# Optimization experiments

Measured on AMD Instinct MI355X. Metric: run time of the kernel, lower is better.

## Reference

```python
import jax, jax.numpy as jnp
import numpy as np

D_MODEL = 1024
N_HEADS = 16
D_K = D_MODEL // N_HEADS  # 64
B, T = 2, 2048


def setup_inputs() -> dict:
    key = jax.random.key(0)
    ks = jax.random.split(key, 6)
    s = 0.02
    x = jax.random.normal(ks[0], (B, T, D_MODEL), dtype=jnp.float32)
    # Stacked per-head projection weights, [H, C, d_k] (no bias, mini-gpt style)
    Wq = jax.random.normal(ks[1], (N_HEADS, D_MODEL, D_K), dtype=jnp.float32) * s
    Wk = jax.random.normal(ks[2], (N_HEADS, D_MODEL, D_K), dtype=jnp.float32) * s
    Wv = jax.random.normal(ks[3], (N_HEADS, D_MODEL, D_K), dtype=jnp.float32) * s
    # Output projection, torch nn.Linear(d_model, d_model): y = x @ Wo.T + bo
    Wo = jax.random.normal(ks[4], (D_MODEL, D_MODEL), dtype=jnp.float32) * s
    bo = jax.random.normal(ks[5], (D_MODEL,), dtype=jnp.float32) * s
    return {"x": x, "Wq": Wq, "Wk": Wk, "Wv": Wv, "Wo": Wo, "bo": bo}


def reference(x, Wq, Wk, Wv, Wo, bo):
    Bq, Tq, C = x.shape
    # Batched per-head projections (replaces the per-head Python loop)
    q = jnp.einsum('btc,hck->bhtk', x, Wq)  # [B,H,T,dk]
    k = jnp.einsum('btc,hck->bhtk', x, Wk)
    v = jnp.einsum('btc,hck->bhtk', x, Wv)
    scale = 1.0 / jnp.sqrt(jnp.asarray(D_K, dtype=x.dtype))
    scores = jnp.einsum('bhtk,bhsk->bhts', q, k) * scale  # [B,H,T,T]
    causal = jnp.tril(jnp.ones((Tq, Tq), dtype=bool))
    scores = jnp.where(causal, scores, jnp.asarray(-1e9, dtype=scores.dtype))
    attn = jax.nn.softmax(scores, axis=-1)
    out = jnp.einsum('bhts,bhsk->bhtk', attn, v)  # [B,H,T,dk]
    # concat heads -> [B,T,C]
    out = out.transpose(0, 2, 1, 3).reshape(Bq, Tq, C)
    return jnp.einsum('btc,dc->btd', out, Wo) + bo
```

## Files before the change

### kernel.cpp

```cpp
#include <hip/hip_runtime.h>
#include <hip/hip_bf16.h>


using short8 = __attribute__((ext_vector_type(8))) short;
using f32x4  = __attribute__((ext_vector_type(4))) float;
using fp16x2 = __attribute__((ext_vector_type(2))) __fp16;
using half4  = __attribute__((ext_vector_type(4))) _Float16;
using half8  = __attribute__((ext_vector_type(8))) _Float16;

#define SCALE_LOG2E 0.18033688011112042f

__device__ __forceinline__ unsigned short f2bf(float f) {
    union { float f; unsigned u; } v; v.f = f;
    unsigned r = v.u + 0x7fffu + ((v.u >> 16) & 1u);
    return (unsigned short)(r >> 16);
}

__device__ __forceinline__ void gld16(const unsigned short* gp, unsigned short* lp) {
    __builtin_amdgcn_global_load_lds(
        (const __attribute__((address_space(1))) void*)(gp),
        (__attribute__((address_space(3))) void*)(unsigned int)(unsigned long long)(lp),
        16, 0, 0);
}

__global__ void prep(const float* __restrict__ x,
                     const float* __restrict__ Wq,
                     const float* __restrict__ Wk,
                     const float* __restrict__ Wv,
                     const float* __restrict__ Wo,
                     unsigned short* __restrict__ xb,
                     unsigned short* __restrict__ wfrag,
                     unsigned short* __restrict__ wofrag) {
    __shared__ float tile[64][65];
    int blk = blockIdx.x;
    int t = threadIdx.x;
    if (blk < 768) {
        int b = blk;
        int cchunk = b & 15;
        int h = (b >> 4) & 15;
        int s = b >> 8;
        const float* W = (s == 0) ? Wq : ((s == 1) ? Wk : Wv);
        float sc = (s == 0) ? SCALE_LOG2E : 1.0f;
        const float* src = W + (h * 1024 + cchunk * 64) * 64;
        #pragma unroll
        for (int it = 0; it < 4; ++it) {
            int idx = (it * 256 + t) * 4;
            int cc = idx >> 6, kk = idx & 63;
            float4 v = *(const float4*)(src + idx);
            tile[cc][kk + 0] = v.x; tile[cc][kk + 1] = v.y;
            tile[cc][kk + 2] = v.z; tile[cc][kk + 3] = v.w;
        }
        __syncthreads();
        int sh = s * 16 + h;
        #pragma unroll
        for (int p = 0; p < 2; ++p) {
            int slot = p * 256 + t;
            int d   = slot & 63;
            int cc8 = slot >> 6;
            int n16  = sh * 4 + (d >> 4);
            int col  = d & 15;
            int kq   = cchunk * 2 + (cc8 >> 2);
            int quad = cc8 & 3;
            ushort4 lo, hi;
            lo.x = f2bf(tile[cc8 * 8 + 0][d] * sc); lo.y = f2bf(tile[cc8 * 8 + 1][d] * sc);
            lo.z = f2bf(tile[cc8 * 8 + 2][d] * sc); lo.w = f2bf(tile[cc8 * 8 + 3][d] * sc);
            hi.x = f2bf(tile[cc8 * 8 + 4][d] * sc); hi.y = f2bf(tile[cc8 * 8 + 5][d] * sc);
            hi.z = f2bf(tile[cc8 * 8 + 6][d] * sc); hi.w = f2bf(tile[cc8 * 8 + 7][d] * sc);
            unsigned short* dst = wfrag + ((size_t)((n16 * 32 + kq) * 64 + quad * 16 + col)) * 8;
            *(ushort4*)dst = lo;
            *(ushort4*)(dst + 4) = hi;
        }
    } else if (blk < 1280) {
        int g = (blk - 768) * 256 + t;
        int col  = g & 15;
        int quad = (g >> 4) & 3;
        int kq   = (g >> 6) & 31;
        int n16  = g >> 11;
        const float* src = Wo + (size_t)(n16 * 16 + col) * 1024 + kq * 32 + quad * 8;
        float4 a = *(const float4*)src;
        float4 b2 = *(const float4*)(src + 4);
        ushort4 lo, hi;
        lo.x = f2bf(a.x); lo.y = f2bf(a.y); lo.z = f2bf(a.z); lo.w = f2bf(a.w);
        hi.x = f2bf(b2.x); hi.y = f2bf(b2.y); hi.z = f2bf(b2.z); hi.w = f2bf(b2.w);
        *(ushort4*)(wofrag + (size_t)g * 8)     = lo;
        *(ushort4*)(wofrag + (size_t)g * 8 + 4) = hi;
    } else {
        int i = (blk - 1280) * 256 + t;
        if (i < 1048576) {
            float4 v = ((const float4*)x)[i];
            ushort4 o;
            o.x = f2bf(v.x); o.y = f2bf(v.y); o.z = f2bf(v.z); o.w = f2bf(v.w);
            ((ushort4*)xb)[i] = o;
        }
    }
}

__global__ __launch_bounds__(128, 4) void qkv_gemm(
        const unsigned short* __restrict__ xb,
        const unsigned short* __restrict__ wtf,
        unsigned short* __restrict__ qB,
        unsigned short* __restrict__ kfrag,
        _Float16* __restrict__ vfrag) {
    __shared__ unsigned short Als[64 * 32];
    int wave = threadIdx.x >> 6;
    int lane = threadIdx.x & 63;
    int col  = lane & 15;
    int quad = lane >> 4;
    int ldr = lane >> 2;
    int ldc = ((lane & 3) ^ ((lane >> 3) & 3)) * 8;
    int swq = (quad ^ ((col >> 1) & 3)) * 8;
    int m0 = blockIdx.x * 64;
    int n0 = blockIdx.y * 128 + wave * 64;
    int n16b = n0 >> 4;
    f32x4 acc[4][4] = {};
    for (int k0 = 0; k0 < 1024; k0 += 32) {
        int kq = k0 >> 5;
        __syncthreads();
        short8 bf[4];
        #pragma unroll
        for (int nb = 0; nb < 4; ++nb)
            bf[nb] = *(const short8*)(wtf +
                ((size_t)((n16b + nb) * 32 + kq) * 64 + lane) * 8);
        #pragma unroll
        for (int j = 0; j < 2; ++j) {
            int row = wave * 32 + j * 16;
            gld16(xb + (size_t)(m0 + row + ldr) * 1024 + k0 + ldc, Als + row * 32);
        }
        __syncthreads();
        short8 af[4];
        #pragma unroll
        for (int i = 0; i < 4; ++i)
            af[i] = *(const short8*)(Als + (i * 16 + col) * 32 + swq);
        #pragma unroll
        for (int mb = 0; mb < 4; ++mb)
            #pragma unroll
            for (int nb = 0; nb < 4; ++nb)
                acc[mb][nb] = __builtin_amdgcn_mfma_f32_16x16x32_bf16(
                    af[mb], bf[nb], acc[mb][nb], 0, 0, 0);
    }
    int sel = blockIdx.y >> 3;
    #pragma unroll
    for (int nb = 0; nb < 4; ++nb) {
        int n = n0 + nb * 16 + col;
        int d10 = n & 1023;
        int h_ = d10 >> 6, d = d10 & 63;
        if (sel == 0) {
            #pragma unroll
            for (int mb = 0; mb < 4; ++mb)
                #pragma unroll
                for (int r = 0; r < 4; ++r) {
                    int m = m0 + mb * 16 + quad * 4 + r;
                    int b_ = m >> 11, t_ = m & 2047;
                    qB[((size_t)(b_ * 16 + h_) * 2048 + t_) * 64 + d] =
                        f2bf(acc[mb][nb][r]);
                }
        } else if (sel == 1) {
            int hK = d >> 5, quadk = (d >> 3) & 3, j = d & 7;
            #pragma unroll
            for (int mb = 0; mb < 4; ++mb)
                #pragma unroll
                for (int r = 0; r < 4; ++r) {
                    int m = m0 + mb * 16 + quad * 4 + r;
                    int b_ = m >> 11, t_ = m & 2047;
                    int bh = b_ * 16 + h_;
                    kfrag[((((size_t)bh * 128 + (t_ >> 4)) * 2 + hK) * 64 +
                           quadk * 16 + (t_ & 15)) * 8 + j] = f2bf(acc[mb][nb][r]);
                }
        } else {
            int nbv = d >> 4, colv = d & 15;
            #pragma unroll
            for (int mb = 0; mb < 4; ++mb) {
                int m = m0 + mb * 16 + quad * 4;
                int b_ = m >> 11, t_ = m & 2047;
                int bh = b_ * 16 + h_;
                half4 hv;
                hv[0] = (_Float16)acc[mb][nb][0]; hv[1] = (_Float16)acc[mb][nb][1];
                hv[2] = (_Float16)acc[mb][nb][2]; hv[3] = (_Float16)acc[mb][nb][3];
                *(half4*)(vfrag + ((((size_t)bh * 64 + (t_ >> 5)) * 4 + nbv) * 64 +
                          ((t_ >> 2) & 3) * 16 + colv) * 8 + ((t_ >> 4) & 1) * 4) = hv;
            }
        }
    }
}

__global__ __launch_bounds__(128, 4) void oproj(
        const unsigned short* __restrict__ A,
        const unsigned short* __restrict__ wof,
        const float* __restrict__ bo,
        float* __restrict__ y) {
    __shared__ unsigned short Als[32 * 32];
    int wave = threadIdx.x >> 6;
    int lane = threadIdx.x & 63;
    int col  = lane & 15;
    int quad = lane >> 4;
    int ldr = lane >> 2;
    int ldc = ((lane & 3) ^ ((lane >> 3) & 3)) * 8;
    int swq = (quad ^ ((col >> 1) & 3)) * 8;
    int m0 = blockIdx.x * 32;
    int n0 = blockIdx.y * 128 + wave * 64;
    int n16b = n0 >> 4;
    f32x4 acc[2][4] = {};
    for (int k0 = 0; k0 < 1024; k0 += 32) {
        int kq = k0 >> 5;
        __syncthreads();
        short8 bf[4];
        #pragma unroll
        for (int nb = 0; nb < 4; ++nb)
            bf[nb] = *(const short8*)(wof +
                ((size_t)((n16b + nb) * 32 + kq) * 64 + lane) * 8);
        gld16(A + (size_t)(m0 + wave * 16 + ldr) * 1024 + k0 + ldc,
              Als + (wave * 16) * 32);
        __syncthreads();
        short8 af[2];
        #pragma unroll
        for (int i = 0; i < 2; ++i)
            af[i] = *(const short8*)(Als + (i * 16 + col) * 32 + swq);
        #pragma unroll
        for (int mb = 0; mb < 2; ++mb)
            #pragma unroll
            for (int nb = 0; nb < 4; ++nb)
                acc[mb][nb] = __builtin_amdgcn_mfma_f32_16x16x32_bf16(
                    af[mb], bf[nb], acc[mb][nb], 0, 0, 0);
    }
    #pragma unroll
    for (int nb = 0; nb < 4; ++nb) {
        int n = n0 + nb * 16 + col;
        float bias = bo[n];
        #pragma unroll
        for (int mb = 0; mb < 2; ++mb)
            #pragma unroll
            for (int r = 0; r < 4; ++r) {
                int m = m0 + mb * 16 + quad * 4 + r;
                y[(size_t)m * 1024 + n] = acc[mb][nb][r] + bias;
            }
    }
}

__global__ __launch_bounds__(256, 3) void attn(
        const unsigned short* __restrict__ qB,
        const unsigned short* __restrict__ kfrag,
        const _Float16* __restrict__ vfrag,
        unsigned short* __restrict__ aout) {
    __shared__ float O_comb[2][64][33];
    __shared__ float L_comb[2][2][2][16];
    int wave = threadIdx.x >> 6;
    int lane = threadIdx.x & 63;
    int col  = lane & 15;
    int quad = lane >> 4;
    int sl     = wave >> 1;
    int parity = wave & 1;
    int bh   = blockIdx.x & 31;
    int pairidx = 31 - (blockIdx.x >> 5);
    int strip = pairidx * 2 + sl;
    int q0 = strip * 32;
    const unsigned short* q = qB + (size_t)bh * 2048 * 64;
    const unsigned short* kf_base = kfrag + (size_t)bh * 128 * 2 * 512;
    const _Float16*       vf_base = vfrag + (size_t)bh * 64 * 4 * 512;

    short8 qf[2][2];
    #pragma unroll
    for (int qb = 0; qb < 2; ++qb)
        #pragma unroll
        for (int h = 0; h < 2; ++h)
            qf[qb][h] = *(const short8*)(q + (size_t)(q0 + qb * 16 + col) * 64 + h * 32 + quad * 8);

    f32x4 o[2][4] = {};
    float l[2] = {0.f, 0.f};

    struct KV { short8 kf[2][2]; half8 vv[4]; };
    KV bufA, bufB;

    auto load_half = [&](int it, int kv32, KV& b) {
        int K16 = it * 4 + kv32 * 2;
        #pragma unroll
        for (int p = 0; p < 2; ++p)
            #pragma unroll
            for (int h = 0; h < 2; ++h)
                b.kf[p][h] = *(const short8*)(kf_base +
                    (((size_t)(K16 + p) * 2 + h) * 64 + lane) * 8);
        #pragma unroll
        for (int nb = 0; nb < 4; ++nb)
            b.vv[nb] = *(const half8*)(vf_base +
                (((size_t)(it * 2 + kv32) * 4 + nb) * 64 + lane) * 8);
    };

    auto compute_half = [&](int it, int kv32, KV& b) {
        int kv0 = it * 64;
        bool diag = (kv0 + 63 > q0);
        #pragma unroll
        for (int par = 0; par < 2; ++par) {
            int kvbase = kv0 + kv32 * 32 + par * 16;
            f32x4 st[2] = {};
            #pragma unroll
            for (int qb = 0; qb < 2; ++qb) {
                st[qb] = __builtin_amdgcn_mfma_f32_16x16x32_bf16(b.kf[par][0], qf[qb][0], st[qb], 0, 0, 0);
                st[qb] = __builtin_amdgcn_mfma_f32_16x16x32_bf16(b.kf[par][1], qf[qb][1], st[qb], 0, 0, 0);
            }
            #pragma unroll
            for (int qb = 0; qb < 2; ++qb) {
                float p0 = __builtin_amdgcn_exp2f(st[qb][0]);
                float p1 = __builtin_amdgcn_exp2f(st[qb][1]);
                float p2 = __builtin_amdgcn_exp2f(st[qb][2]);
                float p3 = __builtin_amdgcn_exp2f(st[qb][3]);
                if (diag) {
                    int qg  = q0 + qb * 16 + col;
                    int kvg = kvbase + quad * 4;
                    p0 = (kvg + 0 > qg) ? 0.f : p0;
                    p1 = (kvg + 1 > qg) ? 0.f : p1;
                    p2 = (kvg + 2 > qg) ? 0.f : p2;
                    p3 = (kvg + 3 > qg) ? 0.f : p3;
                }
                l[qb] += (p0 + p1) + (p2 + p3);
                union { fp16x2 h2[2]; half4 h4; } cvt;
                cvt.h2[0] = __builtin_amdgcn_cvt_pkrtz(p0, p1);
                cvt.h2[1] = __builtin_amdgcn_cvt_pkrtz(p2, p3);
                half4 pf = cvt.h4;
                #pragma unroll
                for (int nb = 0; nb < 4; ++nb) {
                    half4 vf = (par == 0)
                        ? __builtin_shufflevector(b.vv[nb], b.vv[nb], 0, 1, 2, 3)
                        : __builtin_shufflevector(b.vv[nb], b.vv[nb], 4, 5, 6, 7);
                    o[qb][nb] = __builtin_amdgcn_mfma_f32_16x16x16f16(pf, vf, o[qb][nb], 0, 0, 0);
                }
            }
        }
    };

    int n_iter = (q0 + 95) >> 6;
    if (parity < n_iter) load_half(parity, 0, bufA);
    for (int it = parity; it < n_iter; it += 2) {
        load_half(it, 1, bufB);
        compute_half(it, 0, bufA);
        if (it + 2 < n_iter) load_half(it + 2, 0, bufA);
        compute_half(it, 1, bufB);
    }

    #pragma unroll
    for (int qb = 0; qb < 2; ++qb) {
        float lr = l[qb];
        lr += __shfl_xor(lr, 16);
        lr += __shfl_xor(lr, 32);
        l[qb] = lr;
    }
    if (quad == 0) {
        L_comb[sl][parity][0][col] = l[0];
        L_comb[sl][parity][1][col] = l[1];
    }
    if (parity == 1) {
        #pragma unroll
        for (int qb = 0; qb < 2; ++qb)
            #pragma unroll
            for (int nb = 0; nb < 4; ++nb)
                #pragma unroll
                for (int r = 0; r < 4; ++r)
                    O_comb[sl][lane][qb * 16 + nb * 4 + r] = o[qb][nb][r];
    }
    __syncthreads();
    if (parity == 0) {
        int b_ = bh >> 4, h_ = bh & 15;
        #pragma unroll
        for (int qb = 0; qb < 2; ++qb)
            #pragma unroll
            for (int r = 0; r < 4; ++r) {
                int qi = quad * 4 + r;
                float inv_l = 1.0f / (L_comb[sl][0][qb][qi] + L_comb[sl][1][qb][qi]);
                int t_ = q0 + qb * 16 + qi;
                #pragma unroll
                for (int nb = 0; nb < 4; ++nb) {
                    float ov = o[qb][nb][r] + O_comb[sl][lane][qb * 16 + nb * 4 + r];
                    aout[(size_t)(b_ * 2048 + t_) * 1024 + h_ * 64 + nb * 16 + col] =
                        f2bf(ov * inv_l);
                }
            }
    }
}

extern "C" void kernel_launch(void* const* d_in, const int* in_sizes, int n_in,
                              void* d_out, int out_size, void* d_ws, size_t ws_size,
                              hipStream_t stream) {
    const float* x  = (const float*)d_in[0];
    const float* Wq = (const float*)d_in[1];
    const float* Wk = (const float*)d_in[2];
    const float* Wv = (const float*)d_in[3];
    const float* Wo = (const float*)d_in[4];
    const float* bo = (const float*)d_in[5];
    float* y = (float*)d_out;

    unsigned short* xb    = (unsigned short*)d_ws;
    unsigned short* Wtf   = xb    + 4194304;
    unsigned short* Wof   = Wtf   + 3145728;
    unsigned short* qBb   = Wof   + 1048576;
    unsigned short* kfr   = qBb   + 4194304;
    unsigned short* vfr   = kfr   + 4194304;
    unsigned short* aout  = vfr   + 4194304;

    prep<<<5376, 256, 0, stream>>>(x, Wq, Wk, Wv, Wo, xb, Wtf, Wof);
    qkv_gemm<<<dim3(64, 24), 128, 0, stream>>>(xb, Wtf, qBb, kfr, (_Float16*)vfr);
    attn<<<1024, 256, 0, stream>>>(qBb, kfr, (const _Float16*)vfr, aout);
    oproj<<<dim3(128, 8), 128, 0, stream>>>(aout, Wof, bo, y);
}
```

Before: 165.7 us.

## Double K-step per iteration in QKV and output GEMMs; raise MFMA priority in attention

Both projection GEMMs now stage 64-wide K slices in LDS instead of 32, using a new XOR swizzle over 8 chunks. Each iteration loads two sets of B fragments and issues two rounds of MFMAs, which halves the number of barrier pairs and loop iterations. The qkv kernel's launch bound drops from 4 to 3 blocks per SM to make room for the extra registers. Separately, the attention compute section is wrapped in s_setprio(1)/s_setprio(0) so MFMA-heavy waves get scheduling priority. The cost is lower occupancy and more register pressure in the GEMMs.

Result: faster. 162.4 us (-2.0%).

```diff
diff --git a/kernel.cpp b/kernel.cpp
--- a/kernel.cpp
+++ b/kernel.cpp
@@ -95,48 +95,62 @@
     }
 }
 
-__global__ __launch_bounds__(128, 4) void qkv_gemm(
+__global__ __launch_bounds__(128, 3) void qkv_gemm(
         const unsigned short* __restrict__ xb,
         const unsigned short* __restrict__ wtf,
         unsigned short* __restrict__ qB,
         unsigned short* __restrict__ kfrag,
         _Float16* __restrict__ vfrag) {
-    __shared__ unsigned short Als[64 * 32];
+    __shared__ unsigned short Als[64 * 64];
     int wave = threadIdx.x >> 6;
     int lane = threadIdx.x & 63;
     int col  = lane & 15;
     int quad = lane >> 4;
-    int ldr = lane >> 2;
-    int ldc = ((lane & 3) ^ ((lane >> 3) & 3)) * 8;
-    int swq = (quad ^ ((col >> 1) & 3)) * 8;
+    int l8r = lane >> 3;
+    int l8c = lane & 7;
+    int gkc = (l8c ^ l8r) * 8;
     int m0 = blockIdx.x * 64;
     int n0 = blockIdx.y * 128 + wave * 64;
     int n16b = n0 >> 4;
     f32x4 acc[4][4] = {};
-    for (int k0 = 0; k0 < 1024; k0 += 32) {
+    for (int k0 = 0; k0 < 1024; k0 += 64) {
         int kq = k0 >> 5;
         __syncthreads();
-        short8 bf[4];
-        #pragma unroll
-        for (int nb = 0; nb < 4; ++nb)
-            bf[nb] = *(const short8*)(wtf +
+        short8 bf0[4], bf1[4];
+        #pragma unroll
+        for (int nb = 0; nb < 4; ++nb) {
+            bf0[nb] = *(const short8*)(wtf +
                 ((size_t)((n16b + nb) * 32 + kq) * 64 + lane) * 8);
-        #pragma unroll
-        for (int j = 0; j < 2; ++j) {
-            int row = wave * 32 + j * 16;
-            gld16(xb + (size_t)(m0 + row + ldr) * 1024 + k0 + ldc, Als + row * 32);
+            bf1[nb] = *(const short8*)(wtf +
+                ((size_t)((n16b + nb) * 32 + kq + 1) * 64 + lane) * 8);
+        }
+        #pragma unroll
+        for (int j = 0; j < 4; ++j) {
+            int row = wave * 32 + j * 8;
+            gld16(xb + (size_t)(m0 + row + l8r) * 1024 + k0 + gkc, Als + row * 64);
         }
         __syncthreads();
         short8 af[4];
         #pragma unroll
         for (int i = 0; i < 4; ++i)
-            af[i] = *(const short8*)(Als + (i * 16 + col) * 32 + swq);
+            af[i] = *(const short8*)(Als + (i * 16 + col) * 64 +
+                                     ((quad ^ (col & 7)) * 8));
         #pragma unroll
         for (int mb = 0; mb < 4; ++mb)
             #pragma unroll
             for (int nb = 0; nb < 4; ++nb)
                 acc[mb][nb] = __builtin_amdgcn_mfma_f32_16x16x32_bf16(
-                    af[mb], bf[nb], acc[mb][nb], 0, 0, 0);
+                    af[mb], bf0[nb], acc[mb][nb], 0, 0, 0);
+        #pragma unroll
+        for (int i = 0; i < 4; ++i)
+            af[i] = *(const short8*)(Als + (i * 16 + col) * 64 +
+                                     (((quad + 4) ^ (col & 7)) * 8));
+        #pragma unroll
+        for (int mb = 0; mb < 4; ++mb)
+            #pragma unroll
+            for (int nb = 0; nb < 4; ++nb)
+                acc[mb][nb] = __builtin_amdgcn_mfma_f32_16x16x32_bf16(
+                    af[mb], bf1[nb], acc[mb][nb], 0, 0, 0);
     }
     int sel = blockIdx.y >> 3;
     #pragma unroll
@@ -188,39 +202,56 @@
         const unsigned short* __restrict__ wof,
         const float* __restrict__ bo,
         float* __restrict__ y) {
-    __shared__ unsigned short Als[32 * 32];
+    __shared__ unsigned short Als[32 * 64];
     int wave = threadIdx.x >> 6;
     int lane = threadIdx.x & 63;
     int col  = lane & 15;
     int quad = lane >> 4;
-    int ldr = lane >> 2;
-    int ldc = ((lane & 3) ^ ((lane >> 3) & 3)) * 8;
-    int swq = (quad ^ ((col >> 1) & 3)) * 8;
+    int l8r = lane >> 3;
+    int l8c = lane & 7;
+    int gkc = (l8c ^ l8r) * 8;
     int m0 = blockIdx.x * 32;
     int n0 = blockIdx.y * 128 + wave * 64;
     int n16b = n0 >> 4;
     f32x4 acc[2][4] = {};
-    for (int k0 = 0; k0 < 1024; k0 += 32) {
+    for (int k0 = 0; k0 < 1024; k0 += 64) {
         int kq = k0 >> 5;
         __syncthreads();
-        short8 bf[4];
-        #pragma unroll
-        for (int nb = 0; nb < 4; ++nb)
-            bf[nb] = *(const short8*)(wof +
+        short8 bf0[4], bf1[4];
+        #pragma unroll
+        for (int nb = 0; nb < 4; ++nb) {
+            bf0[nb] = *(const short8*)(wof +
                 ((size_t)((n16b + nb) * 32 + kq) * 64 + lane) * 8);
-        gld16(A + (size_t)(m0 + wave * 16 + ldr) * 1024 + k0 + ldc,
-              Als + (wave * 16) * 32);
+            bf1[nb] = *(const short8*)(wof +
+                ((size_t)((n16b + nb) * 32 + kq + 1) * 64 + lane) * 8);
+        }
+        #pragma unroll
+        for (int j = 0; j < 2; ++j) {
+            int row = wave * 16 + j * 8;
+            gld16(A + (size_t)(m0 + row + l8r) * 1024 + k0 + gkc, Als + row * 64);
+        }
         __syncthreads();
         short8 af[2];
         #pragma unroll
         for (int i = 0; i < 2; ++i)
-            af[i] = *(const short8*)(Als + (i * 16 + col) * 32 + swq);
+            af[i] = *(const short8*)(Als + (i * 16 + col) * 64 +
+                                     ((quad ^ (col & 7)) * 8));
         #pragma unroll
         for (int mb = 0; mb < 2; ++mb)
             #pragma unroll
             for (int nb = 0; nb < 4; ++nb)
                 acc[mb][nb] = __builtin_amdgcn_mfma_f32_16x16x32_bf16(
-                    af[mb], bf[nb], acc[mb][nb], 0, 0, 0);
+                    af[mb], bf0[nb], acc[mb][nb], 0, 0, 0);
+        #pragma unroll
+        for (int i = 0; i < 2; ++i)
+            af[i] = *(const short8*)(Als + (i * 16 + col) * 64 +
+                                     (((quad + 4) ^ (col & 7)) * 8));
+        #pragma unroll
+        for (int mb = 0; mb < 2; ++mb)
+            #pragma unroll
+            for (int nb = 0; nb < 4; ++nb)
+                acc[mb][nb] = __builtin_amdgcn_mfma_f32_16x16x32_bf16(
+                    af[mb], bf1[nb], acc[mb][nb], 0, 0, 0);
     }
     #pragma unroll
     for (int nb = 0; nb < 4; ++nb) {
@@ -287,6 +318,7 @@
     auto compute_half = [&](int it, int kv32, KV& b) {
         int kv0 = it * 64;
         bool diag = (kv0 + 63 > q0);
+        __builtin_amdgcn_s_setprio(1);
         #pragma unroll
         for (int par = 0; par < 2; ++par) {
             int kvbase = kv0 + kv32 * 32 + par * 16;
@@ -324,6 +356,7 @@
                 }
             }
         }
+        __builtin_amdgcn_s_setprio(0);
     };
 
     int n_iter = (q0 + 95) >> 6;
```
